# Performance work log

Measured on AMD Instinct MI355X. Metric: run time of the kernel, lower is better.

The kernel has to match this reference:

```python
import jax, jax.numpy as jnp
import numpy as np

B = 32768          # rays
N = 512            # gaussians
NSH = 4            # -> m = 2*NSH+1 = 9 SH coeffs
H = 512.0
W = 512.0
S_MIN = 1.0 / 30.0       # 1 / n_gaussian_max_pixels
S_MAX = 1.0 / 0.75       # 1 / n_gaussian_min_pixels
MU_BORDER = 1.05
PI_APPROX = 3.1416       # matches the literal in the torch source


def setup_inputs() -> dict:
    key = jax.random.key(0)
    ks = jax.random.split(key, 6)
    # pixel coordinates in [0, W) x [0, H)
    x = jax.random.uniform(ks[0], (B, 2), jnp.float32) * jnp.array([W, H], jnp.float32)
    rgbsh = jax.random.uniform(ks[1], (N, 2 * NSH + 1, 3), jnp.float32)
    opacity = jax.random.uniform(ks[2], (N,), jnp.float32)
    mu = jax.random.uniform(ks[3], (N, 2), jnp.float32) * 2.0 - 1.0
    scale = jax.random.uniform(ks[4], (N, 2), jnp.float32)
    angle = jax.random.uniform(ks[5], (N,), jnp.float32) * 2.0 - 1.0
    return {"x": x, "rgbsh": rgbsh, "opacity": opacity,
            "mu": mu, "scale": scale, "angle": angle}


def _forward(x, rgbsh, opacity, mu, scale, angle):
    wh = jnp.array([W, H], x.dtype)                      # (2,)
    xnorm = x / wh * 2.0 - 1.0                           # (B,2) in [-1,1]
    gmu = jnp.tanh(mu) * MU_BORDER                       # (N,2)
    S = jnp.clip(scale, 0.0, 1.0) * (S_MAX - S_MIN) + S_MIN  # (N,2) inverse radii

    # pixel-space offset ray->gaussian: (x - mu)/2 * (w,h)
    vec = (xnorm[:, None, :] - gmu[None, :, :]) * (wh * 0.5)   # (B,N,2)

    # validity mask (computed under no_grad in torch): |S * vec| < 5
    dist = jnp.linalg.norm(vec * S[None], axis=-1)             # (B,N)
    valid = jax.lax.stop_gradient(dist < 5.0)

    # per-gaussian rotation matrices
    alpha = jnp.tanh(angle) * PI_APPROX                        # (N,)
    c, s = jnp.cos(alpha), jnp.sin(alpha)
    R = jnp.stack([jnp.stack([c, -s], -1),
                   jnp.stack([s,  c], -1)], axis=-2)           # (N,2,2)

    # Mahalanobis-like squared distance: || R @ diag(S) @ vec ||^2
    svec = vec * S[None]                                       # (B,N,2)
    rot = jnp.einsum('nij,bnj->bni', R, svec)                  # (B,N,2)
    d2 = jnp.sum(rot * rot, axis=-1)                           # (B,N)

    # view angle in the gaussian frame
    vnorm = vec / (1e-10 + jnp.linalg.norm(vec, axis=-1, keepdims=True))
    vrot = jnp.einsum('nij,bnj->bni', R, vnorm)                # (B,N,2)
    theta = jnp.arctan2(vrot[..., 0], vrot[..., 1])            # (B,N)

    # 2D SH basis: [1, sin(t), cos(t), sin(2t), cos(2t), ...]
    basis = [jnp.ones_like(theta)]
    for i in range(NSH):
        basis.append(jnp.sin(theta * (i + 1)))
        basis.append(jnp.cos(theta * (i + 1)))
    basis = jnp.stack(basis, axis=-1)                          # (B,N,M)

    rgb = jax.nn.sigmoid(jnp.einsum('bnm,nmc->bnc', basis, rgbsh))  # (B,N,3)
    wgt = jnp.where(valid,
                    jnp.exp(-d2) * jax.nn.sigmoid(opacity)[None, :],
                    jnp.zeros((), x.dtype))                    # (B,N)

    # accumulate_along_rays: per-ray weighted sum over gaussians
    return jnp.einsum('bn,bnc->bc', wgt, rgb)                  # (B,3)


def reference(x, rgbsh, opacity, mu, scale, angle):
    return _forward(x, rgbsh, opacity, mu, scale, angle)
```

## Files before the change

kernel.cpp:

```cpp
#include <hip/hip_runtime.h>

#define BDIM 512
#define RPB  64
#define NW   8
#define NG   512


__global__ void pre_kernel(const float* __restrict__ rgbsh,
                           const float* __restrict__ opacity,
                           const float* __restrict__ mu,
                           const float* __restrict__ scale,
                           const float* __restrict__ angle,
                           float4* __restrict__ wsA,
                           float4* __restrict__ wsB,
                           float4* __restrict__ wsSh,
                           int N)
{
    int n = blockIdx.x * blockDim.x + threadIdx.x;
    if (n >= N) return;
    const float S_MIN = 1.0f / 30.0f;
    const float S_MAX = 1.0f / 0.75f;
    float gmx = tanhf(mu[2 * n + 0]) * 1.05f;
    float gmy = tanhf(mu[2 * n + 1]) * 1.05f;
    float Sx = fminf(fmaxf(scale[2 * n + 0], 0.0f), 1.0f) * (S_MAX - S_MIN) + S_MIN;
    float Sy = fminf(fmaxf(scale[2 * n + 1], 0.0f), 1.0f) * (S_MAX - S_MIN) + S_MIN;
    float ax = 256.0f * Sx, ay = 256.0f * Sy;
    wsA[n] = make_float4(ax, ay, -gmx * ax, -gmy * ay);
    float a = tanhf(angle[n]) * 3.1416f;
    float sa, ca;
    sincosf(a, &sa, &ca);
    float w0 = 1.0f / (1.0f + expf(-opacity[n]));
    wsB[n] = make_float4(ca, sa, w0, 1.0f / Sx);
    const float* sh = rgbsh + n * 27;
    float buf[28];
    #pragma unroll
    for (int q = 0; q < 27; ++q) buf[q] = sh[q];
    buf[27] = 1.0f / Sy;
    #pragma unroll
    for (int q = 0; q < 7; ++q)
        wsSh[n * 7 + q] = make_float4(buf[4*q], buf[4*q+1], buf[4*q+2], buf[4*q+3]);
}

__global__ __launch_bounds__(BDIM, 4) void splat_kernel(
    const float*  __restrict__ x,
    const float4* __restrict__ wsA,
    const float4* __restrict__ wsB,
    const float4* __restrict__ wsSh,
    float* __restrict__ out,
    int B)
{
    __shared__ float4 gA[NG];
    __shared__ float4 gB[NG];
    __shared__ float4 gS[NG * 7];
    __shared__ float  acc[NW * RPB * 3];
    const int tid = threadIdx.x;

    if (tid < NG) { gA[tid] = wsA[tid]; gB[tid] = wsB[tid]; }
    #pragma unroll
    for (int i = tid; i < NG * 7; i += BDIM) gS[i] = wsSh[i];
    __syncthreads();

    const int lane = tid & 63;
    const int w    = tid >> 6;
    const int b    = blockIdx.x * RPB + lane;
    const int bb   = (b < B) ? b : (B - 1);
    float2 p2 = *(const float2*)(x + 2 * bb);
    float pnx = p2.x * (1.0f / 256.0f) - 1.0f;
    float pny = p2.y * (1.0f / 256.0f) - 1.0f;

    float accR = 0.0f, accG = 0.0f, accB = 0.0f;
    const int g0 = w * 64;

    for (int j = 0; j < 64; ++j) {
        const int g = g0 + j;
        float4 pa = gA[g];
        float sx = fmaf(pnx, pa.x, pa.z);
        float sy = fmaf(pny, pa.y, pa.w);
        float t  = fmaf(sx, sx, sy * sy);
        bool  v  = t < 25.0f;
        if (__any(v)) {
            if (v) {
                float4 q  = gB[g];
                float4 h6 = gS[g * 7 + 6];
                float c = q.x, s = q.y;
                float rx = fmaf(c, sx, -s * sy);
                float ry = fmaf(s, sx,  c * sy);
                float d2 = fmaf(rx, rx, ry * ry);
                float vx  = sx * q.w;
                float vy  = sy * h6.w;
                float len = sqrtf(fmaf(vx, vx, vy * vy));
                float inv = __builtin_amdgcn_rcpf(1e-10f + len);
                float rvx = fmaf(c, vx, -s * vy);
                float rvy = fmaf(s, vx,  c * vy);
                float s1 = rvx * inv, c1 = rvy * inv;
                float s2 = 2.0f * s1 * c1;
                float c2 = fmaf(c1, c1, -s1 * s1);
                float s3 = fmaf(s2, c1,  c2 * s1);
                float c3 = fmaf(c2, c1, -s2 * s1);
                float s4 = 2.0f * s2 * c2;
                float c4 = fmaf(c2, c2, -s2 * s2);
                float4 h0 = gS[g*7+0], h1 = gS[g*7+1], h2 = gS[g*7+2];
                float4 h3 = gS[g*7+3], h4 = gS[g*7+4], h5 = gS[g*7+5];
                float rr = h0.x, gg = h0.y, bb2 = h0.z;
                rr = fmaf(s1, h0.w, rr);  gg = fmaf(s1, h1.x, gg);  bb2 = fmaf(s1, h1.y, bb2);
                rr = fmaf(c1, h1.z, rr);  gg = fmaf(c1, h1.w, gg);  bb2 = fmaf(c1, h2.x, bb2);
                rr = fmaf(s2, h2.y, rr);  gg = fmaf(s2, h2.z, gg);  bb2 = fmaf(s2, h2.w, bb2);
                rr = fmaf(c2, h3.x, rr);  gg = fmaf(c2, h3.y, gg);  bb2 = fmaf(c2, h3.z, bb2);
                rr = fmaf(s3, h3.w, rr);  gg = fmaf(s3, h4.x, gg);  bb2 = fmaf(s3, h4.y, bb2);
                rr = fmaf(c3, h4.z, rr);  gg = fmaf(c3, h4.w, gg);  bb2 = fmaf(c3, h5.x, bb2);
                rr = fmaf(s4, h5.y, rr);  gg = fmaf(s4, h5.z, gg);  bb2 = fmaf(s4, h5.w, bb2);
                rr = fmaf(c4, h6.x, rr);  gg = fmaf(c4, h6.y, gg);  bb2 = fmaf(c4, h6.z, bb2);
                rr  = __builtin_amdgcn_rcpf(1.0f + __expf(-rr));
                gg  = __builtin_amdgcn_rcpf(1.0f + __expf(-gg));
                bb2 = __builtin_amdgcn_rcpf(1.0f + __expf(-bb2));
                float wt = __expf(-d2) * q.z;
                accR = fmaf(wt, rr,  accR);
                accG = fmaf(wt, gg,  accG);
                accB = fmaf(wt, bb2, accB);
            }
        }
    }

    acc[(w * RPB + lane) * 3 + 0] = accR;
    acc[(w * RPB + lane) * 3 + 1] = accG;
    acc[(w * RPB + lane) * 3 + 2] = accB;
    __syncthreads();
    if (tid < RPB * 3) {
        float s = 0.0f;
        #pragma unroll
        for (int w2 = 0; w2 < NW; ++w2)
            s += acc[w2 * RPB * 3 + tid];
        const int ray = blockIdx.x * RPB + tid / 3;
        if (ray < B)
            out[(size_t)blockIdx.x * RPB * 3 + tid] = s;
    }
}

extern "C" void kernel_launch(void* const* d_in, const int* in_sizes, int n_in,
                              void* d_out, int out_size, void* d_ws, size_t ws_size,
                              hipStream_t stream) {
    const float* x       = (const float*)d_in[0];
    const float* rgbsh   = (const float*)d_in[1];
    const float* opacity = (const float*)d_in[2];
    const float* mu      = (const float*)d_in[3];
    const float* scale   = (const float*)d_in[4];
    const float* angle   = (const float*)d_in[5];
    float* out = (float*)d_out;

    const int B = in_sizes[0] / 2;
    const int N = in_sizes[2];

    char* ws = (char*)d_ws;
    float4* wsA  = (float4*)(ws);
    float4* wsB  = (float4*)(ws + (size_t)N * 16);
    float4* wsSh = (float4*)(ws + (size_t)N * 32);

    pre_kernel<<<(N + 255) / 256, 256, 0, stream>>>(rgbsh, opacity, mu, scale,
                                                    angle, wsA, wsB, wsSh, N);
    splat_kernel<<<(B + RPB - 1) / RPB, BDIM, 0, stream>>>(x, wsA, wsB, wsSh,
                                                           out, B);
}
```

Before: 82.24 us.

## Read SH coefficients via scalar loads and double waves per block

New measurement: 77.16 us. 1.07x faster.

```diff
diff --git a/kernel.cpp b/kernel.cpp
--- a/kernel.cpp
+++ b/kernel.cpp
@@ -1,9 +1,10 @@
 #include <hip/hip_runtime.h>
 
-#define BDIM 512
+#define BDIM 1024
+#define NW   16
 #define RPB  64
-#define NW   8
 #define NG   512
+#define GPW  (NG / NW)
 
 
 __global__ void pre_kernel(const float* __restrict__ rgbsh,
@@ -41,7 +42,7 @@
         wsSh[n * 7 + q] = make_float4(buf[4*q], buf[4*q+1], buf[4*q+2], buf[4*q+3]);
 }
 
-__global__ __launch_bounds__(BDIM, 4) void splat_kernel(
+__global__ __launch_bounds__(BDIM, 8) void splat_kernel(
     const float*  __restrict__ x,
     const float4* __restrict__ wsA,
     const float4* __restrict__ wsB,
@@ -51,13 +52,11 @@
 {
     __shared__ float4 gA[NG];
     __shared__ float4 gB[NG];
-    __shared__ float4 gS[NG * 7];
-    __shared__ float  acc[NW * RPB * 3];
+    __shared__ float  acc[NW][RPB * 3];
     const int tid = threadIdx.x;
 
-    if (tid < NG) { gA[tid] = wsA[tid]; gB[tid] = wsB[tid]; }
-    #pragma unroll
-    for (int i = tid; i < NG * 7; i += BDIM) gS[i] = wsSh[i];
+    if (tid < NG)          gA[tid]      = wsA[tid];
+    else                   gB[tid - NG] = wsB[tid - NG];
     __syncthreads();
 
     const int lane = tid & 63;
@@ -69,9 +68,10 @@
     float pny = p2.y * (1.0f / 256.0f) - 1.0f;
 
     float accR = 0.0f, accG = 0.0f, accB = 0.0f;
-    const int g0 = w * 64;
+    const int g0 = w * GPW;
 
-    for (int j = 0; j < 64; ++j) {
+    #pragma unroll 4
+    for (int j = 0; j < GPW; ++j) {
         const int g = g0 + j;
         float4 pa = gA[g];
         float sx = fmaf(pnx, pa.x, pa.z);
@@ -80,8 +80,10 @@
         bool  v  = t < 25.0f;
         if (__any(v)) {
             if (v) {
-                float4 q  = gB[g];
-                float4 h6 = gS[g * 7 + 6];
+                float4 q = gB[g];
+                const int gu = __builtin_amdgcn_readfirstlane(g);
+                const float4* sh = wsSh + gu * 7;
+                float4 h6 = sh[6];
                 float c = q.x, s = q.y;
                 float rx = fmaf(c, sx, -s * sy);
                 float ry = fmaf(s, sx,  c * sy);
@@ -99,8 +101,8 @@
                 float c3 = fmaf(c2, c1, -s2 * s1);
                 float s4 = 2.0f * s2 * c2;
                 float c4 = fmaf(c2, c2, -s2 * s2);
-                float4 h0 = gS[g*7+0], h1 = gS[g*7+1], h2 = gS[g*7+2];
-                float4 h3 = gS[g*7+3], h4 = gS[g*7+4], h5 = gS[g*7+5];
+                float4 h0 = sh[0], h1 = sh[1], h2 = sh[2];
+                float4 h3 = sh[3], h4 = sh[4], h5 = sh[5];
                 float rr = h0.x, gg = h0.y, bb2 = h0.z;
                 rr = fmaf(s1, h0.w, rr);  gg = fmaf(s1, h1.x, gg);  bb2 = fmaf(s1, h1.y, bb2);
                 rr = fmaf(c1, h1.z, rr);  gg = fmaf(c1, h1.w, gg);  bb2 = fmaf(c1, h2.x, bb2);
@@ -121,18 +123,18 @@
         }
     }
 
-    acc[(w * RPB + lane) * 3 + 0] = accR;
-    acc[(w * RPB + lane) * 3 + 1] = accG;
-    acc[(w * RPB + lane) * 3 + 2] = accB;
+    acc[w][lane * 3 + 0] = accR;
+    acc[w][lane * 3 + 1] = accG;
+    acc[w][lane * 3 + 2] = accB;
     __syncthreads();
     if (tid < RPB * 3) {
         float s = 0.0f;
         #pragma unroll
         for (int w2 = 0; w2 < NW; ++w2)
-            s += acc[w2 * RPB * 3 + tid];
-        const int ray = blockIdx.x * RPB + tid / 3;
-        if (ray < B)
-            out[(size_t)blockIdx.x * RPB * 3 + tid] = s;
+            s += acc[w2][tid];
+        const int idx = blockIdx.x * (RPB * 3) + tid;
+        if (idx < 3 * B)
+            out[idx] = s;
     }
 }
 
```
